# Performance work log

Measured on AMD Instinct MI355X. Metric: run time of the kernel, lower is better.

## Reference

```python
import jax, jax.numpy as jnp
import numpy as np

N_NODES = 100_000
N_EDGES = 1_000_000
D_IN = 64
D_OUT = 64
N_TYPES = 16  # get_options().in_dim; must exceed gate types 9/11 referenced in source


def setup_inputs() -> dict:
    key = jax.random.key(0)
    k = jax.random.split(key, 6)
    feat = jax.random.normal(k[0], (N_NODES, D_IN), dtype=jnp.float32)
    src = jax.random.randint(k[1], (N_EDGES,), 0, N_NODES, dtype=jnp.int32)
    dst = jax.random.randint(k[2], (N_EDGES,), 0, N_NODES, dtype=jnp.int32)
    ntype2 = jax.random.randint(k[3], (N_NODES,), 0, N_TYPES, dtype=jnp.int32)
    # per-type Linear params; xavier-uniform-ish (gain=sqrt(2) for relu)
    limit = np.sqrt(2.0) * np.sqrt(6.0 / (D_IN + D_OUT))
    gate_W = jax.random.uniform(k[4], (N_TYPES, D_IN, D_OUT), jnp.float32, -limit, limit)
    gate_b = jax.random.uniform(k[5], (N_TYPES, D_OUT), jnp.float32, -0.1, 0.1)
    return {"feat": feat, "gate_W": gate_W, "gate_b": gate_b,
            "src": src, "dst": dst, "ntype2": ntype2, "act_flag": 1}


def reference(feat, gate_W, gate_b, src, dst, ntype2, act_flag):
    n = feat.shape[0]
    # update_all(copy_src('h','m'), mean('m','neigh')): gather + segment-mean
    msg = feat[src]                                                  # [E, D_in]
    summed = jax.ops.segment_sum(msg, dst, num_segments=n)           # [N, D_in]
    deg = jax.ops.segment_sum(jnp.ones_like(dst, dtype=feat.dtype), dst, num_segments=n)
    neigh = summed / jnp.maximum(deg, 1.0)[:, None]                  # zero-degree -> 0 (DGL default)
    # apply_nodes_func: route each node through Linear_t with t = ntype2[node]
    # compute all T small GEMMs, then select per node (T is small and fixed)
    out_all = jnp.einsum('nd,tdo->nto', neigh, gate_W) + gate_b[None, :, :]   # [N, T, D_out]
    rst = jnp.take_along_axis(out_all, ntype2.astype(jnp.int32)[:, None, None], axis=1)[:, 0, :]
    # activation is None in this configuration, so act_flag is a no-op
    return rst
```

## Files before the change

kernel.cpp:

```cpp
#include <hip/hip_runtime.h>

#define N_NODES 100000
#define N_EDGES 1000000
#define D 64
#define N_TYPES 16

#define NPB 128
#define NBUCK ((N_NODES + NPB - 1) / NPB)
#define NBLK 512
#define CHUNK 1956
#define NQUAD (CHUNK / 4)
#define ECAP 1520
#define HCAP 1024

#define WS_BCUR  0
#define WS_EBUF  (WS_BCUR + NBUCK * 16)
#define WS_TOTAL (WS_EBUF + NBUCK * ECAP + 64)

__device__ __forceinline__ float lane_bcast(float v, int l) {
    return __uint_as_float(__builtin_amdgcn_readlane(__float_as_uint(v), l));
}

__global__ void __launch_bounds__(512)
place_bucketed(const int* __restrict__ src, const int* __restrict__ dst,
               int* __restrict__ bcur, unsigned* __restrict__ ebuf) {
    __shared__ int hb[NBUCK];
    __shared__ int lo[NBUCK];
    __shared__ int gb[NBUCK];
    __shared__ int cur[NBUCK];
    __shared__ uint2 stage[CHUNK];
    __shared__ int wpart[8];

    int b = blockIdx.x, tid = threadIdx.x;
    int lane = tid & 63, wv = tid >> 6;
    for (int i = tid; i < NBUCK; i += 512) hb[i] = 0;
    __syncthreads();

    int beg = b * CHUNK;
    int e0 = beg + 4 * tid;
    int4 d4 = make_int4(-1, -1, -1, -1);
    if (tid < NQUAD) {
        if (e0 + 3 < N_EDGES) {
            d4 = ((const int4*)(dst + beg))[tid];
        } else if (e0 < N_EDGES) {
            if (e0 + 0 < N_EDGES) d4.x = dst[e0 + 0];
            if (e0 + 1 < N_EDGES) d4.y = dst[e0 + 1];
            if (e0 + 2 < N_EDGES) d4.z = dst[e0 + 2];
            if (e0 + 3 < N_EDGES) d4.w = dst[e0 + 3];
        }
    }
    if (d4.x >= 0) atomicAdd(&hb[d4.x >> 7], 1);
    if (d4.y >= 0) atomicAdd(&hb[d4.y >> 7], 1);
    if (d4.z >= 0) atomicAdd(&hb[d4.z >> 7], 1);
    if (d4.w >= 0) atomicAdd(&hb[d4.w >> 7], 1);
    __syncthreads();

    int i0 = 2 * tid, i1 = 2 * tid + 1;
    int a0 = (i0 < NBUCK) ? hb[i0] : 0;
    int a1 = (i1 < NBUCK) ? hb[i1] : 0;
    int s = a0 + a1;
    int incl = s;
    for (int o = 1; o < 64; o <<= 1) {
        int u = __shfl_up(incl, o, 64);
        if (lane >= o) incl += u;
    }
    if (lane == 63) wpart[wv] = incl;
    __syncthreads();
    if (tid == 0) {
        int r = 0;
        for (int w = 0; w < 8; ++w) { int tmp = wpart[w]; wpart[w] = r; r += tmp; }
    }
    __syncthreads();
    incl += wpart[wv];
    int excl = incl - s;
    if (i0 < NBUCK) { lo[i0] = excl;      cur[i0] = excl; }
    if (i1 < NBUCK) { lo[i1] = excl + a0; cur[i1] = excl + a0; }
    __syncthreads();

    int4 s4 = make_int4(0, 0, 0, 0);
    if (tid < NQUAD && e0 < N_EDGES) {
        if (e0 + 3 < N_EDGES) {
            s4 = ((const int4*)(src + beg))[tid];
        } else {
            if (e0 + 0 < N_EDGES) s4.x = src[e0 + 0];
            if (e0 + 1 < N_EDGES) s4.y = src[e0 + 1];
            if (e0 + 2 < N_EDGES) s4.z = src[e0 + 2];
            if (e0 + 3 < N_EDGES) s4.w = src[e0 + 3];
        }
    }
    if (d4.x >= 0) { int p = atomicAdd(&cur[d4.x >> 7], 1); stage[p] = make_uint2((unsigned)d4.x, (unsigned)s4.x); }
    if (d4.y >= 0) { int p = atomicAdd(&cur[d4.y >> 7], 1); stage[p] = make_uint2((unsigned)d4.y, (unsigned)s4.y); }
    if (d4.z >= 0) { int p = atomicAdd(&cur[d4.z >> 7], 1); stage[p] = make_uint2((unsigned)d4.z, (unsigned)s4.z); }
    if (d4.w >= 0) { int p = atomicAdd(&cur[d4.w >> 7], 1); stage[p] = make_uint2((unsigned)d4.w, (unsigned)s4.w); }

    for (int i = tid; i < NBUCK; i += 512) {
        int c = hb[i];
        if (c > 0) {
            int base = atomicAdd(&bcur[i * 16], c);
            gb[i] = i * ECAP + base - lo[i];
        }
    }
    __syncthreads();

    int end = min(beg + CHUNK, N_EDGES);
    int cnt = end - beg;
    for (int idx = tid; idx < cnt; idx += 512) {
        uint2 v = stage[idx];
        int bk = (int)(v.x >> 7);
        int p = gb[bk] + idx;
        if ((unsigned)(p - bk * ECAP) < ECAP)
            ebuf[p] = ((v.x & (NPB - 1)) << 20) | v.y;
    }
}

__global__ void __launch_bounds__(256)
bucket_gather(const float* __restrict__ feat, const int* __restrict__ bcur,
              const unsigned* __restrict__ ebuf, float* __restrict__ out) {
    __shared__ int hist[64], offL[64], curL[64];
    __shared__ unsigned eL[ECAP];
    __shared__ int sortedL[HCAP];

    int blk = blockIdx.x, tid = threadIdx.x;
    int bucket = blk >> 1, half = blk & 1;
    int ecnt = bcur[bucket * 16];
    if (ecnt > ECAP) ecnt = ECAP;
    int base = bucket * ECAP;
    if (tid < 64) hist[tid] = 0;
    __syncthreads();

    for (int i = tid; i < ecnt; i += 256) {
        unsigned p = ebuf[base + i];
        eL[i] = p;
        if (((p >> 26) & 1u) == (unsigned)half)
            atomicAdd(&hist[(p >> 20) & 63], 1);
    }
    __syncthreads();
    if (tid < 64) {
        int v = hist[tid];
        int incl = v;
        for (int o = 1; o < 64; o <<= 1) {
            int u = __shfl_up(incl, o, 64);
            if (tid >= o) incl += u;
        }
        offL[tid] = incl - v;
        curL[tid] = incl - v;
    }
    __syncthreads();
    for (int i = tid; i < ecnt; i += 256) {
        unsigned p = eL[i];
        if (((p >> 26) & 1u) == (unsigned)half) {
            int pos = atomicAdd(&curL[(p >> 20) & 63], 1);
            if (pos < HCAP) sortedL[pos] = (int)(p & 0xFFFFFu);
        }
    }
    __syncthreads();

    int hw = tid >> 5, h = tid & 31;
    const float2* __restrict__ F = (const float2*)feat;
    int node0 = bucket * NPB + half * 64;
#pragma unroll
    for (int it = 0; it < 8; ++it) {
        int nl = hw * 8 + it;
        int cnt = hist[nl], o = offL[nl];
        float sx = 0.0f, sy = 0.0f;
        int j = 0;
        for (; j + 4 <= cnt; j += 4) {
            int s0 = sortedL[o + j + 0];
            int s1 = sortedL[o + j + 1];
            int s2 = sortedL[o + j + 2];
            int s3 = sortedL[o + j + 3];
            float2 v0 = F[s0 * 32 + h];
            float2 v1 = F[s1 * 32 + h];
            float2 v2 = F[s2 * 32 + h];
            float2 v3 = F[s3 * 32 + h];
            sx += (v0.x + v1.x) + (v2.x + v3.x);
            sy += (v0.y + v1.y) + (v2.y + v3.y);
        }
        for (; j < cnt; ++j) {
            int s = sortedL[o + j];
            float2 v = F[s * 32 + h];
            sx += v.x; sy += v.y;
        }
        int node = node0 + nl;
        if (node < N_NODES) {
            float scale = (cnt > 1) ? (1.0f / (float)cnt) : 1.0f;
            float2 r; r.x = sx * scale; r.y = sy * scale;
            ((float2*)out)[node * 32 + h] = r;
        }
    }
}

__global__ void __launch_bounds__(512, 2)
type_apply(const float* __restrict__ gate_W, const float* __restrict__ gate_b,
           const int* __restrict__ ntype2, float* __restrict__ out) {
    __shared__ unsigned char ord[NPB];
    __shared__ int tc[N_TYPES], tb[N_TYPES], tcur[N_TYPES];

    int k = blockIdx.x, tid = threadIdx.x;
    int lane = tid & 63, wv = tid >> 6;
    int node0 = k * NPB;
    int nvalid = N_NODES - node0; if (nvalid > NPB) nvalid = NPB;

    if (tid < N_TYPES) tc[tid] = 0;
    __syncthreads();
    int myt = -1;
    if (tid < nvalid) { myt = ntype2[node0 + tid]; atomicAdd(&tc[myt], 1); }
    __syncthreads();
    if (tid == 0) {
        int r = 0;
        for (int t = 0; t < N_TYPES; ++t) { tb[t] = r; tcur[t] = r; r += tc[t]; }
    }
    __syncthreads();
    if (tid < nvalid) {
        int p = atomicAdd(&tcur[myt], 1);
        ord[p] = (unsigned char)tid;
    }
    __syncthreads();

    for (int rep = 0; rep < 2; ++rep) {
        int t = wv + rep * 8;
        int cnt = tc[t];
        if (cnt == 0) continue;
        const float* __restrict__ W = gate_W + t * D * D;
        float wreg[D];
#pragma unroll
        for (int d = 0; d < D; ++d) wreg[d] = W[d * D + lane];
        float bias = gate_b[t * D + lane];
        int b0 = tb[t];
        for (int i = 0; i < cnt; ++i) {
            int n = (int)ord[b0 + i];
            float r = out[(node0 + n) * D + lane];
            float a0 = bias, a1 = 0.0f, a2 = 0.0f, a3 = 0.0f;
#pragma unroll
            for (int d = 0; d < D; d += 4) {
                a0 = fmaf(lane_bcast(r, d + 0), wreg[d + 0], a0);
                a1 = fmaf(lane_bcast(r, d + 1), wreg[d + 1], a1);
                a2 = fmaf(lane_bcast(r, d + 2), wreg[d + 2], a2);
                a3 = fmaf(lane_bcast(r, d + 3), wreg[d + 3], a3);
            }
            out[(node0 + n) * D + lane] = (a0 + a1) + (a2 + a3);
        }
    }
}

__global__ void scatter_feat(const float* __restrict__ feat, const int* __restrict__ src,
                             const int* __restrict__ dst, float* __restrict__ accum) {
    long long idx = (long long)blockIdx.x * blockDim.x + threadIdx.x;
    if (idx >= (long long)N_EDGES * D) return;
    int e = (int)(idx >> 6), d = (int)(idx & 63);
    atomicAdd(accum + dst[e] * D + d, feat[src[e] * D + d]);
}
__global__ void scatter_deg(const int* __restrict__ dst, float* __restrict__ deg) {
    int e = blockIdx.x * blockDim.x + threadIdx.x;
    if (e >= N_EDGES) return;
    atomicAdd(deg + dst[e], 1.0f);
}
__global__ void apply_linear(const float* __restrict__ gate_W, const float* __restrict__ gate_b,
                             const int* __restrict__ ntype2, const float* __restrict__ deg,
                             float* __restrict__ out) {
    int node = blockIdx.x * (blockDim.x >> 6) + (threadIdx.x >> 6);
    int lane = threadIdx.x & 63;
    if (node >= N_NODES) return;
    int t = ntype2[node];
    float dv = deg[node]; dv = dv > 1.0f ? dv : 1.0f;
    float nv = out[node * D + lane] / dv;
    const float* W = gate_W + t * D * D;
    float acc = gate_b[t * D + lane];
#pragma unroll 16
    for (int d = 0; d < D; ++d)
        acc = fmaf(__shfl(nv, d, 64), W[d * D + lane], acc);
    out[node * D + lane] = acc;
}

extern "C" void kernel_launch(void* const* d_in, const int* in_sizes, int n_in,
                              void* d_out, int out_size, void* d_ws, size_t ws_size,
                              hipStream_t stream) {
    const float* feat   = (const float*)d_in[0];
    const float* gate_W = (const float*)d_in[1];
    const float* gate_b = (const float*)d_in[2];
    const int*   src    = (const int*)d_in[3];
    const int*   dst    = (const int*)d_in[4];
    const int*   ntype2 = (const int*)d_in[5];
    float* out = (float*)d_out;

    if (ws_size >= (size_t)WS_TOTAL * 4) {
        int* ws = (int*)d_ws;
        int* bcur      = ws + WS_BCUR;
        unsigned* ebuf = (unsigned*)(ws + WS_EBUF);

        hipMemsetAsync(bcur, 0, sizeof(int) * NBUCK * 16, stream);
        place_bucketed<<<NBLK, 512, 0, stream>>>(src, dst, bcur, ebuf);
        bucket_gather<<<NBUCK * 2, 256, 0, stream>>>(feat, bcur, ebuf, out);
        type_apply<<<NBUCK, 512, 0, stream>>>(gate_W, gate_b, ntype2, out);
    } else {
        float* deg = (float*)d_ws;
        hipMemsetAsync(out, 0, sizeof(float) * N_NODES * D, stream);
        hipMemsetAsync(deg, 0, sizeof(float) * N_NODES, stream);
        long long total = (long long)N_EDGES * D;
        scatter_feat<<<(int)((total + 255) / 256), 256, 0, stream>>>(feat, src, dst, out);
        scatter_deg<<<(N_EDGES + 255) / 256, 256, 0, stream>>>(dst, deg);
        apply_linear<<<(N_NODES + 3) / 4, 256, 0, stream>>>(gate_W, gate_b, ntype2, deg, out);
    }
}
```

Baseline: 190.3 us.

## Bucket edges into coarse 512-node regions and balance type_apply across waves

The edge partition now uses 196 coarse regions of 512 destination nodes instead of 782 buckets of 128. This gives fewer global atomics and larger contiguous writes in the placement kernel. Each gather block handles 64 nodes and scans its whole region's edges twice, filtering by window, instead of staging a smaller bucket in shared memory. That cuts LDS use but multiplies global reads of the edge buffer about fourfold. The per-type apply now gives each wave a fixed 16-node slice of the type-sorted order and reloads weights only when the type changes, which balances work across waves at the cost of more weight reloads.

Result: no change. 189.1 us (-0.7%).

```diff
diff --git a/kernel.cpp b/kernel.cpp
--- a/kernel.cpp
+++ b/kernel.cpp
@@ -5,59 +5,58 @@
 #define D 64
 #define N_TYPES 16
 
+#define NC 196
+#define CNODES 512
+#define PBLK 512
+#define CHUNK 1956
+#define NQUAD (CHUNK / 4)
+#define RCAP 5504
 #define NPB 128
 #define NBUCK ((N_NODES + NPB - 1) / NPB)
-#define NBLK 512
-#define CHUNK 1956
-#define NQUAD (CHUNK / 4)
-#define ECAP 1520
-#define HCAP 1024
-
-#define WS_BCUR  0
-#define WS_EBUF  (WS_BCUR + NBUCK * 16)
-#define WS_TOTAL (WS_EBUF + NBUCK * ECAP + 64)
+#define GBLK ((N_NODES + 63) / 64)
+#define SCAP 1024
+
+#define WS_CCUR  0
+#define WS_EBUF  (WS_CCUR + NC * 16 + 64)
+#define WS_TOTAL (WS_EBUF + NC * RCAP + 64)
 
 __device__ __forceinline__ float lane_bcast(float v, int l) {
     return __uint_as_float(__builtin_amdgcn_readlane(__float_as_uint(v), l));
 }
 
 __global__ void __launch_bounds__(512)
-place_bucketed(const int* __restrict__ src, const int* __restrict__ dst,
-               int* __restrict__ bcur, unsigned* __restrict__ ebuf) {
-    __shared__ int hb[NBUCK];
-    __shared__ int lo[NBUCK];
-    __shared__ int gb[NBUCK];
-    __shared__ int cur[NBUCK];
+place_coarse(const int* __restrict__ src, const int* __restrict__ dst,
+             int* __restrict__ ccur, unsigned* __restrict__ ebuf) {
+    __shared__ int hb[NC], lo[NC], gb[NC], cur[NC];
     __shared__ uint2 stage[CHUNK];
     __shared__ int wpart[8];
 
     int b = blockIdx.x, tid = threadIdx.x;
     int lane = tid & 63, wv = tid >> 6;
-    for (int i = tid; i < NBUCK; i += 512) hb[i] = 0;
+    for (int i = tid; i < NC; i += 512) hb[i] = 0;
     __syncthreads();
 
     int beg = b * CHUNK;
     int e0 = beg + 4 * tid;
     int4 d4 = make_int4(-1, -1, -1, -1);
-    if (tid < NQUAD) {
+    if (tid < NQUAD && e0 < N_EDGES) {
         if (e0 + 3 < N_EDGES) {
             d4 = ((const int4*)(dst + beg))[tid];
-        } else if (e0 < N_EDGES) {
-            if (e0 + 0 < N_EDGES) d4.x = dst[e0 + 0];
+        } else {
+            d4.x = dst[e0];
             if (e0 + 1 < N_EDGES) d4.y = dst[e0 + 1];
             if (e0 + 2 < N_EDGES) d4.z = dst[e0 + 2];
-            if (e0 + 3 < N_EDGES) d4.w = dst[e0 + 3];
-        }
-    }
-    if (d4.x >= 0) atomicAdd(&hb[d4.x >> 7], 1);
-    if (d4.y >= 0) atomicAdd(&hb[d4.y >> 7], 1);
-    if (d4.z >= 0) atomicAdd(&hb[d4.z >> 7], 1);
-    if (d4.w >= 0) atomicAdd(&hb[d4.w >> 7], 1);
+        }
+    }
+    if (d4.x >= 0) atomicAdd(&hb[d4.x >> 9], 1);
+    if (d4.y >= 0) atomicAdd(&hb[d4.y >> 9], 1);
+    if (d4.z >= 0) atomicAdd(&hb[d4.z >> 9], 1);
+    if (d4.w >= 0) atomicAdd(&hb[d4.w >> 9], 1);
     __syncthreads();
 
     int i0 = 2 * tid, i1 = 2 * tid + 1;
-    int a0 = (i0 < NBUCK) ? hb[i0] : 0;
-    int a1 = (i1 < NBUCK) ? hb[i1] : 0;
+    int a0 = (i0 < NC) ? hb[i0] : 0;
+    int a1 = (i1 < NC) ? hb[i1] : 0;
     int s = a0 + a1;
     int incl = s;
     for (int o = 1; o < 64; o <<= 1) {
@@ -68,13 +67,13 @@
     __syncthreads();
     if (tid == 0) {
         int r = 0;
-        for (int w = 0; w < 8; ++w) { int tmp = wpart[w]; wpart[w] = r; r += tmp; }
+        for (int w = 0; w < 8; ++w) { int t = wpart[w]; wpart[w] = r; r += t; }
     }
     __syncthreads();
     incl += wpart[wv];
     int excl = incl - s;
-    if (i0 < NBUCK) { lo[i0] = excl;      cur[i0] = excl; }
-    if (i1 < NBUCK) { lo[i1] = excl + a0; cur[i1] = excl + a0; }
+    if (i0 < NC) { lo[i0] = excl;      cur[i0] = excl; }
+    if (i1 < NC) { lo[i1] = excl + a0; cur[i1] = excl + a0; }
     __syncthreads();
 
     int4 s4 = make_int4(0, 0, 0, 0);
@@ -82,22 +81,25 @@
         if (e0 + 3 < N_EDGES) {
             s4 = ((const int4*)(src + beg))[tid];
         } else {
-            if (e0 + 0 < N_EDGES) s4.x = src[e0 + 0];
+            s4.x = src[e0];
             if (e0 + 1 < N_EDGES) s4.y = src[e0 + 1];
             if (e0 + 2 < N_EDGES) s4.z = src[e0 + 2];
-            if (e0 + 3 < N_EDGES) s4.w = src[e0 + 3];
-        }
-    }
-    if (d4.x >= 0) { int p = atomicAdd(&cur[d4.x >> 7], 1); stage[p] = make_uint2((unsigned)d4.x, (unsigned)s4.x); }
-    if (d4.y >= 0) { int p = atomicAdd(&cur[d4.y >> 7], 1); stage[p] = make_uint2((unsigned)d4.y, (unsigned)s4.y); }
-    if (d4.z >= 0) { int p = atomicAdd(&cur[d4.z >> 7], 1); stage[p] = make_uint2((unsigned)d4.z, (unsigned)s4.z); }
-    if (d4.w >= 0) { int p = atomicAdd(&cur[d4.w >> 7], 1); stage[p] = make_uint2((unsigned)d4.w, (unsigned)s4.w); }
-
-    for (int i = tid; i < NBUCK; i += 512) {
+        }
+    }
+    if (d4.x >= 0) { int c = d4.x >> 9; int p = atomicAdd(&cur[c], 1);
+                     stage[p] = make_uint2((unsigned)c, ((unsigned)(d4.x & 511) << 17) | (unsigned)s4.x); }
+    if (d4.y >= 0) { int c = d4.y >> 9; int p = atomicAdd(&cur[c], 1);
+                     stage[p] = make_uint2((unsigned)c, ((unsigned)(d4.y & 511) << 17) | (unsigned)s4.y); }
+    if (d4.z >= 0) { int c = d4.z >> 9; int p = atomicAdd(&cur[c], 1);
+                     stage[p] = make_uint2((unsigned)c, ((unsigned)(d4.z & 511) << 17) | (unsigned)s4.z); }
+    if (d4.w >= 0) { int c = d4.w >> 9; int p = atomicAdd(&cur[c], 1);
+                     stage[p] = make_uint2((unsigned)c, ((unsigned)(d4.w & 511) << 17) | (unsigned)s4.w); }
+
+    for (int i = tid; i < NC; i += 512) {
         int c = hb[i];
         if (c > 0) {
-            int base = atomicAdd(&bcur[i * 16], c);
-            gb[i] = i * ECAP + base - lo[i];
+            int base = atomicAdd(&ccur[i * 16], c);
+            gb[i] = i * RCAP + base - lo[i];
         }
     }
     __syncthreads();
@@ -106,33 +108,32 @@
     int cnt = end - beg;
     for (int idx = tid; idx < cnt; idx += 512) {
         uint2 v = stage[idx];
-        int bk = (int)(v.x >> 7);
-        int p = gb[bk] + idx;
-        if ((unsigned)(p - bk * ECAP) < ECAP)
-            ebuf[p] = ((v.x & (NPB - 1)) << 20) | v.y;
+        int p = gb[v.x] + idx;
+        if ((unsigned)(p - v.x * RCAP) < RCAP)
+            ebuf[p] = v.y;
     }
 }
 
 __global__ void __launch_bounds__(256)
-bucket_gather(const float* __restrict__ feat, const int* __restrict__ bcur,
+bucket_gather(const float* __restrict__ feat, const int* __restrict__ ccur,
               const unsigned* __restrict__ ebuf, float* __restrict__ out) {
     __shared__ int hist[64], offL[64], curL[64];
-    __shared__ unsigned eL[ECAP];
-    __shared__ int sortedL[HCAP];
+    __shared__ int sortedL[SCAP];
 
     int blk = blockIdx.x, tid = threadIdx.x;
-    int bucket = blk >> 1, half = blk & 1;
-    int ecnt = bcur[bucket * 16];
-    if (ecnt > ECAP) ecnt = ECAP;
-    int base = bucket * ECAP;
+    int node0 = blk * 64;
+    unsigned reg = (unsigned)(node0 >> 9);
+    unsigned wnd = (unsigned)((node0 >> 6) & 7);
+    int rcnt = ccur[reg * 16];
+    if (rcnt > RCAP) rcnt = RCAP;
+    int rbase = (int)reg * RCAP;
     if (tid < 64) hist[tid] = 0;
     __syncthreads();
 
-    for (int i = tid; i < ecnt; i += 256) {
-        unsigned p = ebuf[base + i];
-        eL[i] = p;
-        if (((p >> 26) & 1u) == (unsigned)half)
-            atomicAdd(&hist[(p >> 20) & 63], 1);
+    for (int i = tid; i < rcnt; i += 256) {
+        unsigned p = ebuf[rbase + i];
+        if ((p >> 23) == wnd)
+            atomicAdd(&hist[(p >> 17) & 63], 1);
     }
     __syncthreads();
     if (tid < 64) {
@@ -146,18 +147,17 @@
         curL[tid] = incl - v;
     }
     __syncthreads();
-    for (int i = tid; i < ecnt; i += 256) {
-        unsigned p = eL[i];
-        if (((p >> 26) & 1u) == (unsigned)half) {
-            int pos = atomicAdd(&curL[(p >> 20) & 63], 1);
-            if (pos < HCAP) sortedL[pos] = (int)(p & 0xFFFFFu);
+    for (int i = tid; i < rcnt; i += 256) {
+        unsigned p = ebuf[rbase + i];
+        if ((p >> 23) == wnd) {
+            int pos = atomicAdd(&curL[(p >> 17) & 63], 1);
+            if (pos < SCAP) sortedL[pos] = (int)(p & 0x1FFFFu);
         }
     }
     __syncthreads();
 
     int hw = tid >> 5, h = tid & 31;
     const float2* __restrict__ F = (const float2*)feat;
-    int node0 = bucket * NPB + half * 64;
 #pragma unroll
     for (int it = 0; it < 8; ++it) {
         int nl = hw * 8 + it;
@@ -194,7 +194,8 @@
 type_apply(const float* __restrict__ gate_W, const float* __restrict__ gate_b,
            const int* __restrict__ ntype2, float* __restrict__ out) {
     __shared__ unsigned char ord[NPB];
-    __shared__ int tc[N_TYPES], tb[N_TYPES], tcur[N_TYPES];
+    __shared__ unsigned char typ[NPB];
+    __shared__ int tc[N_TYPES], tcur[N_TYPES];
 
     int k = blockIdx.x, tid = threadIdx.x;
     int lane = tid & 63, wv = tid >> 6;
@@ -208,38 +209,40 @@
     __syncthreads();
     if (tid == 0) {
         int r = 0;
-        for (int t = 0; t < N_TYPES; ++t) { tb[t] = r; tcur[t] = r; r += tc[t]; }
+        for (int t = 0; t < N_TYPES; ++t) { int cc = tc[t]; tcur[t] = r; r += cc; }
     }
     __syncthreads();
     if (tid < nvalid) {
         int p = atomicAdd(&tcur[myt], 1);
         ord[p] = (unsigned char)tid;
-    }
-    __syncthreads();
-
-    for (int rep = 0; rep < 2; ++rep) {
-        int t = wv + rep * 8;
-        int cnt = tc[t];
-        if (cnt == 0) continue;
-        const float* __restrict__ W = gate_W + t * D * D;
-        float wreg[D];
+        typ[p] = (unsigned char)myt;
+    }
+    __syncthreads();
+
+    int i0 = wv * 16, i1 = i0 + 16; if (i1 > nvalid) i1 = nvalid;
+    int tprev = -1;
+    float wreg[D];
+    float bias = 0.0f;
+    for (int i = i0; i < i1; ++i) {
+        int n = (int)ord[i];
+        int t = (int)typ[i];
+        if (t != tprev) {
+            tprev = t;
+            const float* __restrict__ W = gate_W + t * D * D;
 #pragma unroll
-        for (int d = 0; d < D; ++d) wreg[d] = W[d * D + lane];
-        float bias = gate_b[t * D + lane];
-        int b0 = tb[t];
-        for (int i = 0; i < cnt; ++i) {
-            int n = (int)ord[b0 + i];
-            float r = out[(node0 + n) * D + lane];
-            float a0 = bias, a1 = 0.0f, a2 = 0.0f, a3 = 0.0f;
+            for (int d = 0; d < D; ++d) wreg[d] = W[d * D + lane];
+            bias = gate_b[t * D + lane];
+        }
+        float r = out[(node0 + n) * D + lane];
+        float a0 = bias, a1 = 0.0f, a2 = 0.0f, a3 = 0.0f;
 #pragma unroll
-            for (int d = 0; d < D; d += 4) {
-                a0 = fmaf(lane_bcast(r, d + 0), wreg[d + 0], a0);
-                a1 = fmaf(lane_bcast(r, d + 1), wreg[d + 1], a1);
-                a2 = fmaf(lane_bcast(r, d + 2), wreg[d + 2], a2);
-                a3 = fmaf(lane_bcast(r, d + 3), wreg[d + 3], a3);
-            }
-            out[(node0 + n) * D + lane] = (a0 + a1) + (a2 + a3);
-        }
+        for (int d = 0; d < D; d += 4) {
+            a0 = fmaf(lane_bcast(r, d + 0), wreg[d + 0], a0);
+            a1 = fmaf(lane_bcast(r, d + 1), wreg[d + 1], a1);
+            a2 = fmaf(lane_bcast(r, d + 2), wreg[d + 2], a2);
+            a3 = fmaf(lane_bcast(r, d + 3), wreg[d + 3], a3);
+        }
+        out[(node0 + n) * D + lane] = (a0 + a1) + (a2 + a3);
     }
 }
 
@@ -285,12 +288,12 @@
 
     if (ws_size >= (size_t)WS_TOTAL * 4) {
         int* ws = (int*)d_ws;
-        int* bcur      = ws + WS_BCUR;
+        int* ccur      = ws + WS_CCUR;
         unsigned* ebuf = (unsigned*)(ws + WS_EBUF);
 
-        hipMemsetAsync(bcur, 0, sizeof(int) * NBUCK * 16, stream);
-        place_bucketed<<<NBLK, 512, 0, stream>>>(src, dst, bcur, ebuf);
-        bucket_gather<<<NBUCK * 2, 256, 0, stream>>>(feat, bcur, ebuf, out);
+        hipMemsetAsync(ccur, 0, sizeof(int) * NC * 16, stream);
+        place_coarse<<<PBLK, 512, 0, stream>>>(src, dst, ccur, ebuf);
+        bucket_gather<<<GBLK, 256, 0, stream>>>(feat, ccur, ebuf, out);
         type_apply<<<NBUCK, 512, 0, stream>>>(gate_W, gate_b, ntype2, out);
     } else {
         float* deg = (float*)d_ws;
```

## Reorganize type_apply into per-type blocks over large node windows

Applied to the files above, without the earlier changes.

type_apply now assigns each block one node type and a 2048-node window, instead of one block per 128-node bucket that loops over all 16 types. Each block builds a shared list of matching nodes, loads that type's weight column into registers once, and spreads the matching nodes across its 8 waves. This amortizes the per-wave 64-float weight load over many more nodes, cutting repeated weight reads from L2. In exchange, ntype2 is scanned 16 times and the list is capped at 256 entries, so an unusually dense type in a window would silently drop nodes. Small tail-load cleanups in place_bucketed accompany the change.

Result: faster. 184.4 us (-3.1%).

```diff
diff --git a/kernel.cpp b/kernel.cpp
--- a/kernel.cpp
+++ b/kernel.cpp
@@ -12,6 +12,10 @@
 #define NQUAD (CHUNK / 4)
 #define ECAP 1520
 #define HCAP 1024
+
+#define AWIN 2048
+#define ABLKS ((N_NODES + AWIN - 1) / AWIN)
+#define LCAP 256
 
 #define WS_BCUR  0
 #define WS_EBUF  (WS_BCUR + NBUCK * 16)
@@ -39,14 +43,13 @@
     int beg = b * CHUNK;
     int e0 = beg + 4 * tid;
     int4 d4 = make_int4(-1, -1, -1, -1);
-    if (tid < NQUAD) {
+    if (tid < NQUAD && e0 < N_EDGES) {
         if (e0 + 3 < N_EDGES) {
             d4 = ((const int4*)(dst + beg))[tid];
-        } else if (e0 < N_EDGES) {
-            if (e0 + 0 < N_EDGES) d4.x = dst[e0 + 0];
+        } else {
+            d4.x = dst[e0];
             if (e0 + 1 < N_EDGES) d4.y = dst[e0 + 1];
             if (e0 + 2 < N_EDGES) d4.z = dst[e0 + 2];
-            if (e0 + 3 < N_EDGES) d4.w = dst[e0 + 3];
         }
     }
     if (d4.x >= 0) atomicAdd(&hb[d4.x >> 7], 1);
@@ -68,7 +71,7 @@
     __syncthreads();
     if (tid == 0) {
         int r = 0;
-        for (int w = 0; w < 8; ++w) { int tmp = wpart[w]; wpart[w] = r; r += tmp; }
+        for (int w = 0; w < 8; ++w) { int t = wpart[w]; wpart[w] = r; r += t; }
     }
     __syncthreads();
     incl += wpart[wv];
@@ -82,10 +85,9 @@
         if (e0 + 3 < N_EDGES) {
             s4 = ((const int4*)(src + beg))[tid];
         } else {
-            if (e0 + 0 < N_EDGES) s4.x = src[e0 + 0];
+            s4.x = src[e0];
             if (e0 + 1 < N_EDGES) s4.y = src[e0 + 1];
             if (e0 + 2 < N_EDGES) s4.z = src[e0 + 2];
-            if (e0 + 3 < N_EDGES) s4.w = src[e0 + 3];
         }
     }
     if (d4.x >= 0) { int p = atomicAdd(&cur[d4.x >> 7], 1); stage[p] = make_uint2((unsigned)d4.x, (unsigned)s4.x); }
@@ -193,53 +195,43 @@
 __global__ void __launch_bounds__(512, 2)
 type_apply(const float* __restrict__ gate_W, const float* __restrict__ gate_b,
            const int* __restrict__ ntype2, float* __restrict__ out) {
-    __shared__ unsigned char ord[NPB];
-    __shared__ int tc[N_TYPES], tb[N_TYPES], tcur[N_TYPES];
-
-    int k = blockIdx.x, tid = threadIdx.x;
-    int lane = tid & 63, wv = tid >> 6;
-    int node0 = k * NPB;
-    int nvalid = N_NODES - node0; if (nvalid > NPB) nvalid = NPB;
-
-    if (tid < N_TYPES) tc[tid] = 0;
-    __syncthreads();
-    int myt = -1;
-    if (tid < nvalid) { myt = ntype2[node0 + tid]; atomicAdd(&tc[myt], 1); }
-    __syncthreads();
-    if (tid == 0) {
-        int r = 0;
-        for (int t = 0; t < N_TYPES; ++t) { tb[t] = r; tcur[t] = r; r += tc[t]; }
-    }
-    __syncthreads();
-    if (tid < nvalid) {
-        int p = atomicAdd(&tcur[myt], 1);
-        ord[p] = (unsigned char)tid;
-    }
-    __syncthreads();
-
-    for (int rep = 0; rep < 2; ++rep) {
-        int t = wv + rep * 8;
-        int cnt = tc[t];
-        if (cnt == 0) continue;
-        const float* __restrict__ W = gate_W + t * D * D;
-        float wreg[D];
+    __shared__ int list[LCAP];
+    __shared__ int lcnt;
+
+    int tid = threadIdx.x, lane = tid & 63, wv = tid >> 6;
+    int t = blockIdx.x & 15;
+    int n0 = (blockIdx.x >> 4) * AWIN;
+    if (tid == 0) lcnt = 0;
+    __syncthreads();
+    for (int i = tid; i < AWIN; i += 512) {
+        int n = n0 + i;
+        if (n < N_NODES && ntype2[n] == t) {
+            int p = atomicAdd(&lcnt, 1);
+            if (p < LCAP) list[p] = n;
+        }
+    }
+    __syncthreads();
+    int cnt = min(lcnt, LCAP);
+    if (cnt == 0) return;
+
+    const float* __restrict__ W = gate_W + t * D * D;
+    float wreg[D];
 #pragma unroll
-        for (int d = 0; d < D; ++d) wreg[d] = W[d * D + lane];
-        float bias = gate_b[t * D + lane];
-        int b0 = tb[t];
-        for (int i = 0; i < cnt; ++i) {
-            int n = (int)ord[b0 + i];
-            float r = out[(node0 + n) * D + lane];
-            float a0 = bias, a1 = 0.0f, a2 = 0.0f, a3 = 0.0f;
+    for (int d = 0; d < D; ++d) wreg[d] = W[d * D + lane];
+    float bias = gate_b[t * D + lane];
+
+    for (int i = wv; i < cnt; i += 8) {
+        int n = list[i];
+        float r = out[n * D + lane];
+        float a0 = bias, a1 = 0.0f, a2 = 0.0f, a3 = 0.0f;
 #pragma unroll
-            for (int d = 0; d < D; d += 4) {
-                a0 = fmaf(lane_bcast(r, d + 0), wreg[d + 0], a0);
-                a1 = fmaf(lane_bcast(r, d + 1), wreg[d + 1], a1);
-                a2 = fmaf(lane_bcast(r, d + 2), wreg[d + 2], a2);
-                a3 = fmaf(lane_bcast(r, d + 3), wreg[d + 3], a3);
-            }
-            out[(node0 + n) * D + lane] = (a0 + a1) + (a2 + a3);
-        }
+        for (int d = 0; d < D; d += 4) {
+            a0 = fmaf(lane_bcast(r, d + 0), wreg[d + 0], a0);
+            a1 = fmaf(lane_bcast(r, d + 1), wreg[d + 1], a1);
+            a2 = fmaf(lane_bcast(r, d + 2), wreg[d + 2], a2);
+            a3 = fmaf(lane_bcast(r, d + 3), wreg[d + 3], a3);
+        }
+        out[n * D + lane] = (a0 + a1) + (a2 + a3);
     }
 }
 
@@ -291,7 +283,7 @@
         hipMemsetAsync(bcur, 0, sizeof(int) * NBUCK * 16, stream);
         place_bucketed<<<NBLK, 512, 0, stream>>>(src, dst, bcur, ebuf);
         bucket_gather<<<NBUCK * 2, 256, 0, stream>>>(feat, bcur, ebuf, out);
-        type_apply<<<NBUCK, 512, 0, stream>>>(gate_W, gate_b, ntype2, out);
+        type_apply<<<ABLKS * 16, 512, 0, stream>>>(gate_W, gate_b, ntype2, out);
     } else {
         float* deg = (float*)d_ws;
         hipMemsetAsync(out, 0, sizeof(float) * N_NODES * D, stream);
```
